# Optimization experiments

Measured on AMD Instinct MI355X. Metric: run time of the kernel, lower is better.

## Reference

```python
import jax, jax.numpy as jnp
import numpy as np

B, T, D, NH, L = 8192, 100, 44, 64, 8  # batch, seq/ode steps, obs_dim, rnn hidden, latent


def setup_inputs() -> dict:
    key = jax.random.key(0)
    ks = jax.random.split(key, 12)
    s = 0.1
    return {
        "x": jax.random.normal(ks[0], (B, T, D), jnp.float32),
        "mask": jax.random.randint(ks[1], (B, T, D), 0, 2).astype(jnp.float32),
        "epsilon": jax.random.normal(ks[2], (B, L), jnp.float32),
        "Wi2h": jax.random.normal(ks[3], (D + NH, NH), jnp.float32) * s,
        "bi2h": jnp.zeros((NH,), jnp.float32),
        "Wh2o": jax.random.normal(ks[4], (NH, 2 * L), jnp.float32) * s,
        "bh2o": jnp.zeros((2 * L,), jnp.float32),
        "Wf1": jax.random.normal(ks[5], (L, NH), jnp.float32) * s,
        "bf1": jnp.zeros((NH,), jnp.float32),
        "Wf2": jax.random.normal(ks[6], (NH, NH), jnp.float32) * s,
        "bf2": jnp.zeros((NH,), jnp.float32),
        "Wf3": jax.random.normal(ks[7], (NH, L), jnp.float32) * s,
        "bf3": jnp.zeros((L,), jnp.float32),
        "Wd1": jax.random.normal(ks[8], (L, NH), jnp.float32) * s,
        "bd1": jnp.zeros((NH,), jnp.float32),
        "Wd2": jax.random.normal(ks[9], (NH, D), jnp.float32) * s,
        "bd2": jnp.zeros((D,), jnp.float32),
    }


def reference(x, mask, epsilon, Wi2h, bi2h, Wh2o, bh2o,
              Wf1, bf1, Wf2, bf2, Wf3, bf3, Wd1, bd1, Wd2, bd2):
    masked_x = x * mask  # [B,T,D]

    # --- reverse-time recognition RNN (scan over time, reversed) ---
    def rnn_step(h, obs):
        h = jnp.tanh(jnp.concatenate([obs, h], axis=1) @ Wi2h + bi2h)
        return h, None

    xs_rev = jnp.transpose(masked_x[:, ::-1, :], (1, 0, 2))  # [T,B,D]
    h0 = jnp.zeros((x.shape[0], Wi2h.shape[1]), x.dtype)
    h_final, _ = jax.lax.scan(rnn_step, h0, xs_rev)
    out = h_final @ Wh2o + bh2o  # [B,2L]
    qz0_mean, qz0_logvar = out[:, :L], out[:, L:]

    # reparameterized latent sample
    z0 = epsilon * jnp.exp(0.5 * qz0_logvar) + qz0_mean  # [B,L]

    # --- latent ODE dynamics, fixed-step RK4 over ts = linspace(0,1,100) ---
    def f(z):
        h1 = jax.nn.elu(z @ Wf1 + bf1)
        h2 = jax.nn.elu(h1 @ Wf2 + bf2)
        return h2 @ Wf3 + bf3

    dt = jnp.asarray(1.0 / (T - 1), x.dtype)

    def rk4_step(z, _):
        k1 = f(z)
        k2 = f(z + 0.5 * dt * k1)
        k3 = f(z + 0.5 * dt * k2)
        k4 = f(z + dt * k3)
        zn = z + (dt / 6.0) * (k1 + 2.0 * k2 + 2.0 * k3 + k4)
        return zn, zn

    _, zs = jax.lax.scan(rk4_step, z0, None, length=T - 1)  # [T-1,B,L]
    pred_z = jnp.transpose(jnp.concatenate([z0[None], zs], axis=0), (1, 0, 2))  # [B,T,L]

    # --- decoder ---
    pred_x = jax.nn.relu(pred_z @ Wd1 + bd1) @ Wd2 + bd2  # [B,T,D]

    # fill observed entries back in
    updated_x = jnp.where(masked_x != 0, masked_x, pred_x)

    # --- loss ---
    noise_logvar = 2.0 * jnp.log(jnp.asarray(0.3, x.dtype))
    log2pi = jnp.log(jnp.asarray(2.0 * np.pi, x.dtype))
    logpx = (-0.5 * (log2pi + noise_logvar +
                     (x - updated_x) ** 2 / jnp.exp(noise_logvar))).sum((-1, -2))  # [B]
    kl = (-0.5 * qz0_logvar + (jnp.exp(qz0_logvar) + qz0_mean ** 2) / 2.0 - 0.5).sum(-1)  # [B]
    loss = jnp.mean(-logpx + kl)
    return loss
```

## Files before the change

kernel.cpp:

```cpp
#include <hip/hip_runtime.h>
#include <stdint.h>


constexpr int B_ = 8192, T_ = 100, D_ = 44, NH_ = 64, L_ = 8;

typedef float f32x4 __attribute__((ext_vector_type(4)));
typedef uint32_t u32x2 __attribute__((ext_vector_type(2)));

#if __has_builtin(__builtin_amdgcn_mfma_f32_16x16x16bf16_1k)
typedef short frag16 __attribute__((ext_vector_type(4)));
#define MFMA16(a, b, c) __builtin_amdgcn_mfma_f32_16x16x16bf16_1k(a, b, c, 0, 0, 0)
#define USE_F16 0
#elif __has_builtin(__builtin_amdgcn_mfma_f32_16x16x16_bf16_1k)
typedef short frag16 __attribute__((ext_vector_type(4)));
#define MFMA16(a, b, c) __builtin_amdgcn_mfma_f32_16x16x16_bf16_1k(a, b, c, 0, 0, 0)
#define USE_F16 0
#elif __has_builtin(__builtin_amdgcn_mfma_f32_16x16x16_bf16)
typedef __bf16 frag16 __attribute__((ext_vector_type(4)));
#define MFMA16(a, b, c) __builtin_amdgcn_mfma_f32_16x16x16_bf16(a, b, c, 0, 0, 0)
#define USE_F16 0
#else
typedef _Float16 frag16 __attribute__((ext_vector_type(4)));
#define MFMA16(a, b, c) __builtin_amdgcn_mfma_f32_16x16x16f16(a, b, c, 0, 0, 0)
#define USE_F16 1
#endif

__device__ __forceinline__ float fexp2(float x) { return __builtin_amdgcn_exp2f(x); }
__device__ __forceinline__ float frcp(float x) { return __builtin_amdgcn_rcpf(x); }
__device__ __forceinline__ float fexp(float x) { return fexp2(x * 1.44269504088896341f); }
__device__ __forceinline__ float tanh_f(float x) {
  float e = fexp2(x * 2.88539008177792681f);
  return 1.0f - 2.0f * frcp(e + 1.0f);
}
__device__ __forceinline__ float elu_f(float x) { return x > 0.0f ? x : (fexp(x) - 1.0f); }

__device__ __forceinline__ uint32_t EW(float v) {
#if USE_F16
  return (uint32_t)__builtin_bit_cast(unsigned short, (_Float16)v);
#else
  return (uint32_t)__builtin_bit_cast(unsigned short, (__bf16)v);
#endif
}
__device__ __forceinline__ uint32_t PK2(float lo, float hi) { return EW(lo) | (EW(hi) << 16); }
__device__ __forceinline__ frag16 fr4(float a, float b, float c, float d) {
  u32x2 u = {PK2(a, b), PK2(c, d)};
  return __builtin_bit_cast(frag16, u);
}
__device__ __forceinline__ frag16 frpk(f32x4 v) {
  u32x2 u = {PK2(v[0], v[1]), PK2(v[2], v[3])};
  return __builtin_bit_cast(frag16, u);
}
__device__ __forceinline__ float f4get(const float4& f, int i) {
  return i == 0 ? f.x : (i == 1 ? f.y : (i == 2 ? f.z : f.w));
}

__global__ __launch_bounds__(128) void fused_kernel(
    const float* __restrict__ x, const float* __restrict__ mask,
    const float* __restrict__ eps,
    const float* __restrict__ Wi2h, const float* __restrict__ bi2h,
    const float* __restrict__ Wh2o, const float* __restrict__ bh2o,
    const float* __restrict__ Wf1, const float* __restrict__ bf1,
    const float* __restrict__ Wf2, const float* __restrict__ bf2,
    const float* __restrict__ Wf3, const float* __restrict__ bf3,
    const float* __restrict__ Wd1, const float* __restrict__ bd1,
    const float* __restrict__ Wd2, const float* __restrict__ bd2,
    float* __restrict__ part) {
  const int tid = threadIdx.x;
  const int wid = tid >> 6;
  const int lane = tid & 63;
  const int c = lane & 15, q = lane >> 4;
  const int r0 = blockIdx.x * 16;
  const f32x4 fzero = {0.f, 0.f, 0.f, 0.f};

  __shared__ __align__(16) uint32_t ring[6400];
  __shared__ uint32_t flags[104];
  __shared__ float sse_sh;

  if (tid < 104) flags[tid] = 0u;
  __syncthreads();

  float klt = 0.0f;

  if (wid == 0) {
    const frag16 fgbias = fr4(1.0f, 0.f, 0.f, 0.f);

    frag16 Ai[4][7];
#pragma unroll
    for (int tau = 0; tau < 4; ++tau)
#pragma unroll
      for (int kc = 0; kc < 7; ++kc) {
        const int m = 16 * tau + c;
        float wv[4];
#pragma unroll
        for (int i = 0; i < 4; ++i) {
          const int k = 16 * kc + 4 * q + i;
          float v = 0.0f;
          if (k < 64) v = Wi2h[(44 + k) * 64 + m];
          else if (k < 108) v = Wi2h[(k - 64) * 64 + m];
          else if (k == 108) v = bi2h[m];
          wv[i] = v;
        }
        Ai[tau][kc] = fr4(wv[0], wv[1], wv[2], wv[3]);
      }
    frag16 Ah2o[4];
#pragma unroll
    for (int kc = 0; kc < 4; ++kc) {
      float wv[4];
#pragma unroll
      for (int i = 0; i < 4; ++i) wv[i] = Wh2o[(16 * kc + 4 * q + i) * 16 + c];
      Ah2o[kc] = fr4(wv[0], wv[1], wv[2], wv[3]);
    }
    f32x4 bo;
#pragma unroll
    for (int r = 0; r < 4; ++r) bo[r] = bh2o[4 * q + r];

    const float* xrowbase = x + (size_t)(r0 + c) * T_ * D_;
    const float* mrowbase = mask + (size_t)(r0 + c) * T_ * D_;

    auto load_obs = [&](int t, float4* xv, float4* mv) {
      const float* xp = xrowbase + (size_t)t * D_;
      const float* mp = mrowbase + (size_t)t * D_;
      xv[0] = *(const float4*)(xp + 4 * q);
      mv[0] = *(const float4*)(mp + 4 * q);
      xv[1] = *(const float4*)(xp + 16 + 4 * q);
      mv[1] = *(const float4*)(mp + 16 + 4 * q);
      float4 zz = {0.f, 0.f, 0.f, 0.f};
      xv[2] = zz; mv[2] = zz;
      if (q < 3) {
        xv[2] = *(const float4*)(xp + 32 + 4 * q);
        mv[2] = *(const float4*)(mp + 32 + 4 * q);
      }
    };
    auto make_ob = [&](const float4* cx, const float4* cm, frag16* ob) {
#pragma unroll
      for (int j = 0; j < 2; ++j) {
        u32x2 u = {PK2(cx[j].x * cm[j].x, cx[j].y * cm[j].y),
                   PK2(cx[j].z * cm[j].z, cx[j].w * cm[j].w)};
        ob[j] = __builtin_bit_cast(frag16, u);
      }
      u32x2 u = {PK2(cx[2].x * cm[2].x, cx[2].y * cm[2].y),
                 PK2(cx[2].z * cm[2].z, cx[2].w * cm[2].w)};
      ob[2] = (q < 3) ? __builtin_bit_cast(frag16, u) : fgbias;
    };

    f32x4 hc[4] = {};
    float4 xo[3], mo[3];
    load_obs(T_ - 1, xo, mo);
    frag16 ob[3];
    make_ob(xo, mo, ob);
    f32x4 pC[4];
#pragma unroll
    for (int tau = 0; tau < 4; ++tau)
      pC[tau] = MFMA16(Ai[tau][6], ob[2],
                       MFMA16(Ai[tau][5], ob[1],
                              MFMA16(Ai[tau][4], ob[0], fzero)));

#pragma unroll 1
    for (int s = 0; s < T_; ++s) {
      const int t = T_ - 1 - s;
      if (t > 0) load_obs(t - 1, xo, mo);

      frag16 bh[4];
#pragma unroll
      for (int tau = 0; tau < 4; ++tau) bh[tau] = frpk(hc[tau]);
#pragma unroll
      for (int tau = 0; tau < 4; ++tau) {
        f32x4 p0 = MFMA16(Ai[tau][0], bh[0], pC[tau]);
        f32x4 p1 = MFMA16(Ai[tau][1], bh[1], fzero);
        f32x4 p2 = MFMA16(Ai[tau][2], bh[2], fzero);
        f32x4 p3 = MFMA16(Ai[tau][3], bh[3], fzero);
#pragma unroll
        for (int r = 0; r < 4; ++r)
          hc[tau][r] = tanh_f((p0[r] + p1[r]) + (p2[r] + p3[r]));
      }

      if (t > 0) {
        make_ob(xo, mo, ob);
#pragma unroll
        for (int tau = 0; tau < 4; ++tau)
          pC[tau] = MFMA16(Ai[tau][6], ob[2],
                           MFMA16(Ai[tau][5], ob[1],
                                  MFMA16(Ai[tau][4], ob[0], fzero)));
      }
    }

    frag16 bhF[4];
#pragma unroll
    for (int tau = 0; tau < 4; ++tau) bhF[tau] = frpk(hc[tau]);
    f32x4 o = bo;
#pragma unroll
    for (int kc = 0; kc < 4; ++kc) o = MFMA16(Ah2o[kc], bhF[kc], o);

    float lv[4];
#pragma unroll
    for (int r = 0; r < 4; ++r)
      lv[r] = __int_as_float(__shfl(__float_as_int(o[r]), lane + 32, 64));

    f32x4 z = {};
    if (q < 2) {
      const float4 ev = *(const float4*)(eps + (size_t)(r0 + c) * 8 + 4 * q);
#pragma unroll
      for (int r = 0; r < 4; ++r) {
        const float m = o[r];
        z[r] = f4get(ev, r) * fexp(0.5f * lv[r]) + m;
        klt += -0.5f * lv[r] + (fexp(lv[r]) + m * m) * 0.5f - 0.5f;
      }
    }
    klt += __shfl_xor(klt, 1);  klt += __shfl_xor(klt, 2);
    klt += __shfl_xor(klt, 4);  klt += __shfl_xor(klt, 8);
    klt += __shfl_xor(klt, 16); klt += __shfl_xor(klt, 32);

    __builtin_amdgcn_sched_barrier(0);

    frag16 A1[4], A2[4][4], A3[4];
#pragma unroll
    for (int tau = 0; tau < 4; ++tau) {
      float w1[4];
#pragma unroll
      for (int i = 0; i < 4; ++i) {
        const int k = 4 * q + i;
        w1[i] = k < 8 ? Wf1[k * 64 + 16 * tau + c] : (k == 8 ? bf1[16 * tau + c] : 0.0f);
      }
      A1[tau] = fr4(w1[0], w1[1], w1[2], w1[3]);
    }
#pragma unroll
    for (int tau = 0; tau < 4; ++tau)
#pragma unroll
      for (int kc = 0; kc < 4; ++kc) {
        float wv[4];
#pragma unroll
        for (int i = 0; i < 4; ++i) wv[i] = Wf2[(16 * kc + 4 * q + i) * 64 + 16 * tau + c];
        A2[tau][kc] = fr4(wv[0], wv[1], wv[2], wv[3]);
      }
#pragma unroll
    for (int kc = 0; kc < 4; ++kc) {
      float wv[4];
#pragma unroll
      for (int i = 0; i < 4; ++i)
        wv[i] = (c < 8) ? Wf3[(16 * kc + 4 * q + i) * 8 + c] : 0.0f;
      A3[kc] = fr4(wv[0], wv[1], wv[2], wv[3]);
    }
    f32x4 b2_[4], b3_;
#pragma unroll
    for (int tau = 0; tau < 4; ++tau)
#pragma unroll
      for (int r = 0; r < 4; ++r) b2_[tau][r] = bf2[16 * tau + 4 * q + r];
#pragma unroll
    for (int r = 0; r < 4; ++r) b3_[r] = (q < 2) ? bf3[4 * q + r] : 0.0f;

    auto build_bz = [&](f32x4 zv) -> frag16 {
      u32x2 u = {PK2(zv[0], zv[1]), PK2(zv[2], zv[3])};
      if (q == 2) { u[0] = EW(1.0f); u[1] = 0u; }
      else if (q == 3) { u[0] = 0u; u[1] = 0u; }
      return __builtin_bit_cast(frag16, u);
    };

    auto feval = [&](frag16 bz) -> f32x4 {
      frag16 bh[4];
#pragma unroll
      for (int tau = 0; tau < 4; ++tau) {
        f32x4 h = MFMA16(A1[tau], bz, fzero);
#pragma unroll
        for (int r = 0; r < 4; ++r) h[r] = elu_f(h[r]);
        bh[tau] = frpk(h);
      }
      frag16 bg[4];
#pragma unroll
      for (int tau = 0; tau < 4; ++tau) {
        f32x4 g0 = MFMA16(A2[tau][0], bh[0], b2_[tau]);
        f32x4 g1 = MFMA16(A2[tau][1], bh[1], fzero);
        f32x4 g2 = MFMA16(A2[tau][2], bh[2], fzero);
        f32x4 g3 = MFMA16(A2[tau][3], bh[3], fzero);
        f32x4 g;
#pragma unroll
        for (int r = 0; r < 4; ++r) g[r] = elu_f((g0[r] + g1[r]) + (g2[r] + g3[r]));
        bg[tau] = frpk(g);
      }
      f32x4 r0_ = MFMA16(A3[0], bg[0], b3_);
      f32x4 r1_ = MFMA16(A3[1], bg[1], fzero);
      f32x4 r2_ = MFMA16(A3[2], bg[2], fzero);
      f32x4 r3_ = MFMA16(A3[3], bg[3], fzero);
      f32x4 rr;
#pragma unroll
      for (int r = 0; r < 4; ++r) rr[r] = (r0_[r] + r1_[r]) + (r2_[r] + r3_[r]);
      return rr;
    };

    const float dt = 1.0f / (float)(T_ - 1);
    const float hdt = 0.5f * dt;

#pragma unroll 1
    for (int t = 0; t < T_; ++t) {
      if (q < 2) {
        u32x2 v = {PK2(z[0], z[1]), PK2(z[2], z[3])};
        *(u32x2*)(ring + (t * 32 + c * 2 + q) * 2) = v;
      }
      asm volatile("" ::: "memory");
      if (lane == 0) ((volatile uint32_t*)flags)[t] = 1u;

      if (t < T_ - 1) {
        f32x4 k1 = feval(build_bz(z));
        f32x4 zt;
#pragma unroll
        for (int r = 0; r < 4; ++r) zt[r] = z[r] + hdt * k1[r];
        f32x4 k2 = feval(build_bz(zt));
#pragma unroll
        for (int r = 0; r < 4; ++r) zt[r] = z[r] + hdt * k2[r];
        f32x4 k3 = feval(build_bz(zt));
#pragma unroll
        for (int r = 0; r < 4; ++r) zt[r] = z[r] + dt * k3[r];
        f32x4 k4 = feval(build_bz(zt));
#pragma unroll
        for (int r = 0; r < 4; ++r)
          z[r] += (dt / 6.0f) * (k1[r] + 2.0f * (k2[r] + k3[r]) + k4[r]);
      }
    }
  } else {
    frag16 Ad1[4], Ad2[3][4];
#pragma unroll
    for (int tau = 0; tau < 4; ++tau) {
      float wd[4];
#pragma unroll
      for (int i = 0; i < 4; ++i) {
        const int k = 4 * q + i;
        wd[i] = k < 8 ? Wd1[k * 64 + 16 * tau + c] : (k == 8 ? bd1[16 * tau + c] : 0.0f);
      }
      Ad1[tau] = fr4(wd[0], wd[1], wd[2], wd[3]);
    }
#pragma unroll
    for (int tau = 0; tau < 3; ++tau)
#pragma unroll
      for (int kc = 0; kc < 4; ++kc) {
        const int m = 16 * tau + c;
        float wv[4];
#pragma unroll
        for (int i = 0; i < 4; ++i)
          wv[i] = (m < 44) ? Wd2[(16 * kc + 4 * q + i) * 44 + m] : 0.0f;
        Ad2[tau][kc] = fr4(wv[0], wv[1], wv[2], wv[3]);
      }
    f32x4 bd2_[3];
#pragma unroll
    for (int tau = 0; tau < 3; ++tau)
#pragma unroll
      for (int r = 0; r < 4; ++r) {
        const int d = 16 * tau + 4 * q + r;
        bd2_[tau][r] = (d < 44) ? bd2[d] : 0.0f;
      }

    float qacc = 0.0f;
    volatile uint32_t* vf = flags;

#pragma unroll 1
    for (int t = 0; t < T_; ++t) {
      float4 xc[3], mc[3];
#pragma unroll
      for (int tau = 0; tau < 3; ++tau) {
        const int d0 = 16 * tau + 4 * q;
        if (d0 < 44) {
          const size_t off = (size_t)(r0 + c) * T_ * D_ + (size_t)t * D_ + d0;
          xc[tau] = *(const float4*)(x + off);
          mc[tau] = *(const float4*)(mask + off);
        } else {
          float4 zz = {0.f, 0.f, 0.f, 0.f};
          xc[tau] = zz; mc[tau] = zz;
        }
      }

      while (vf[t] == 0u) __builtin_amdgcn_s_sleep(1);
      asm volatile("" ::: "memory");

      frag16 bz;
      {
        u32x2 u = {0u, 0u};
        if (q < 2) u = *(const u32x2*)(ring + (t * 32 + c * 2 + q) * 2);
        else if (q == 2) u[0] = EW(1.0f);
        bz = __builtin_bit_cast(frag16, u);
      }

      frag16 bhd[4];
#pragma unroll
      for (int tau = 0; tau < 4; ++tau) {
        f32x4 hd = MFMA16(Ad1[tau], bz, fzero);
#pragma unroll
        for (int r = 0; r < 4; ++r) hd[r] = fmaxf(hd[r], 0.0f);
        bhd[tau] = frpk(hd);
      }
#pragma unroll
      for (int tau = 0; tau < 3; ++tau) {
        f32x4 p0 = MFMA16(Ad2[tau][0], bhd[0], bd2_[tau]);
        f32x4 p1 = MFMA16(Ad2[tau][1], bhd[1], fzero);
        f32x4 p2 = MFMA16(Ad2[tau][2], bhd[2], fzero);
        f32x4 p3 = MFMA16(Ad2[tau][3], bhd[3], fzero);
        if (16 * tau + 4 * q < 44) {
#pragma unroll
          for (int r = 0; r < 4; ++r) {
            const float p = (p0[r] + p1[r]) + (p2[r] + p3[r]);
            const float xa = f4get(xc[tau], r), ma = f4get(mc[tau], r);
            const float mx = xa * ma;
            const float upd = (mx != 0.0f) ? mx : p;
            const float df = xa - upd;
            qacc += df * df;
          }
        }
      }
    }

    float tot = qacc * (0.5f / 0.09f);
    tot += __shfl_xor(tot, 1);  tot += __shfl_xor(tot, 2);
    tot += __shfl_xor(tot, 4);  tot += __shfl_xor(tot, 8);
    tot += __shfl_xor(tot, 16); tot += __shfl_xor(tot, 32);
    if (lane == 0) sse_sh = tot;
  }

  __syncthreads();
  if (tid == 0) part[blockIdx.x] = sse_sh + klt;
}

__global__ __launch_bounds__(512) void reduce_kernel(const float* __restrict__ part,
                                                     float* __restrict__ out) {
  __shared__ float s[8];
  const int tid = threadIdx.x;
  float v = part[tid];
  v += __shfl_xor(v, 1);  v += __shfl_xor(v, 2);
  v += __shfl_xor(v, 4);  v += __shfl_xor(v, 8);
  v += __shfl_xor(v, 16); v += __shfl_xor(v, 32);
  if ((tid & 63) == 0) s[tid >> 6] = v;
  __syncthreads();
  if (tid == 0) {
    float acc = 0.0f;
#pragma unroll
    for (int i = 0; i < 8; ++i) acc += s[i];
    const float c0 = 0.28503427112126353f;
    out[0] = acc * (1.0f / (float)B_) - (float)(T_ * D_) * c0;
  }
}

extern "C" void kernel_launch(void* const* d_in, const int* in_sizes, int n_in,
                              void* d_out, int out_size, void* d_ws, size_t ws_size,
                              hipStream_t stream) {
  const float* x    = (const float*)d_in[0];
  const float* mask = (const float*)d_in[1];
  const float* eps  = (const float*)d_in[2];
  const float* Wi2h = (const float*)d_in[3];
  const float* bi2h = (const float*)d_in[4];
  const float* Wh2o = (const float*)d_in[5];
  const float* bh2o = (const float*)d_in[6];
  const float* Wf1  = (const float*)d_in[7];
  const float* bf1  = (const float*)d_in[8];
  const float* Wf2  = (const float*)d_in[9];
  const float* bf2  = (const float*)d_in[10];
  const float* Wf3  = (const float*)d_in[11];
  const float* bf3  = (const float*)d_in[12];
  const float* Wd1  = (const float*)d_in[13];
  const float* bd1  = (const float*)d_in[14];
  const float* Wd2  = (const float*)d_in[15];
  const float* bd2  = (const float*)d_in[16];

  float* loss = (float*)d_out;
  float* part = (float*)d_ws;

  fused_kernel<<<dim3(B_ / 16), dim3(128), 0, stream>>>(
      x, mask, eps, Wi2h, bi2h, Wh2o, bh2o, Wf1, bf1, Wf2, bf2, Wf3, bf3,
      Wd1, bd1, Wd2, bd2, part);
  reduce_kernel<<<dim3(1), dim3(512), 0, stream>>>(part, loss);
}
```

Before: 698.1 us.

## Process two 16-row tiles per block to interleave independent MFMA chains

```diff
diff --git a/kernel.cpp b/kernel.cpp
--- a/kernel.cpp
+++ b/kernel.cpp
@@ -69,10 +69,10 @@
   const int wid = tid >> 6;
   const int lane = tid & 63;
   const int c = lane & 15, q = lane >> 4;
-  const int r0 = blockIdx.x * 16;
+  const int r0 = blockIdx.x * 32;
   const f32x4 fzero = {0.f, 0.f, 0.f, 0.f};
 
-  __shared__ __align__(16) uint32_t ring[6400];
+  __shared__ __align__(16) uint32_t ring[12800];
   __shared__ uint32_t flags[104];
   __shared__ float sse_sh;
 
@@ -114,12 +114,16 @@
 #pragma unroll
     for (int r = 0; r < 4; ++r) bo[r] = bh2o[4 * q + r];
 
-    const float* xrowbase = x + (size_t)(r0 + c) * T_ * D_;
-    const float* mrowbase = mask + (size_t)(r0 + c) * T_ * D_;
-
-    auto load_obs = [&](int t, float4* xv, float4* mv) {
-      const float* xp = xrowbase + (size_t)t * D_;
-      const float* mp = mrowbase + (size_t)t * D_;
+    const float* xrb[2], * mrb[2];
+#pragma unroll
+    for (int it = 0; it < 2; ++it) {
+      xrb[it] = x + (size_t)(r0 + 16 * it + c) * T_ * D_;
+      mrb[it] = mask + (size_t)(r0 + 16 * it + c) * T_ * D_;
+    }
+
+    auto load_obs = [&](int it, int t, float4* xv, float4* mv) {
+      const float* xp = xrb[it] + (size_t)t * D_;
+      const float* mp = mrb[it] + (size_t)t * D_;
       xv[0] = *(const float4*)(xp + 4 * q);
       mv[0] = *(const float4*)(mp + 4 * q);
       xv[1] = *(const float4*)(xp + 16 + 4 * q);
@@ -143,68 +147,93 @@
       ob[2] = (q < 3) ? __builtin_bit_cast(frag16, u) : fgbias;
     };
 
-    f32x4 hc[4] = {};
-    float4 xo[3], mo[3];
-    load_obs(T_ - 1, xo, mo);
-    frag16 ob[3];
-    make_ob(xo, mo, ob);
-    f32x4 pC[4];
+    f32x4 hc[2][4] = {};
+    float4 xo[2][3], mo[2][3];
+    frag16 ob[2][3];
+    f32x4 pC[2][4];
+#pragma unroll
+    for (int it = 0; it < 2; ++it) {
+      load_obs(it, T_ - 1, xo[it], mo[it]);
+      make_ob(xo[it], mo[it], ob[it]);
+    }
 #pragma unroll
     for (int tau = 0; tau < 4; ++tau)
-      pC[tau] = MFMA16(Ai[tau][6], ob[2],
-                       MFMA16(Ai[tau][5], ob[1],
-                              MFMA16(Ai[tau][4], ob[0], fzero)));
+#pragma unroll
+      for (int it = 0; it < 2; ++it)
+        pC[it][tau] = MFMA16(Ai[tau][6], ob[it][2],
+                             MFMA16(Ai[tau][5], ob[it][1],
+                                    MFMA16(Ai[tau][4], ob[it][0], fzero)));
 
 #pragma unroll 1
     for (int s = 0; s < T_; ++s) {
       const int t = T_ - 1 - s;
-      if (t > 0) load_obs(t - 1, xo, mo);
-
-      frag16 bh[4];
-#pragma unroll
-      for (int tau = 0; tau < 4; ++tau) bh[tau] = frpk(hc[tau]);
+      if (t > 0) {
+#pragma unroll
+        for (int it = 0; it < 2; ++it) load_obs(it, t - 1, xo[it], mo[it]);
+      }
+
+      frag16 bh[2][4];
+#pragma unroll
+      for (int tau = 0; tau < 4; ++tau)
+#pragma unroll
+        for (int it = 0; it < 2; ++it) bh[it][tau] = frpk(hc[it][tau]);
 #pragma unroll
       for (int tau = 0; tau < 4; ++tau) {
-        f32x4 p0 = MFMA16(Ai[tau][0], bh[0], pC[tau]);
-        f32x4 p1 = MFMA16(Ai[tau][1], bh[1], fzero);
-        f32x4 p2 = MFMA16(Ai[tau][2], bh[2], fzero);
-        f32x4 p3 = MFMA16(Ai[tau][3], bh[3], fzero);
-#pragma unroll
-        for (int r = 0; r < 4; ++r)
-          hc[tau][r] = tanh_f((p0[r] + p1[r]) + (p2[r] + p3[r]));
+        f32x4 p0[2], p1[2], p2[2], p3[2];
+#pragma unroll
+        for (int it = 0; it < 2; ++it) p0[it] = MFMA16(Ai[tau][0], bh[it][0], pC[it][tau]);
+#pragma unroll
+        for (int it = 0; it < 2; ++it) p1[it] = MFMA16(Ai[tau][1], bh[it][1], fzero);
+#pragma unroll
+        for (int it = 0; it < 2; ++it) p2[it] = MFMA16(Ai[tau][2], bh[it][2], fzero);
+#pragma unroll
+        for (int it = 0; it < 2; ++it) p3[it] = MFMA16(Ai[tau][3], bh[it][3], fzero);
+#pragma unroll
+        for (int it = 0; it < 2; ++it)
+#pragma unroll
+          for (int r = 0; r < 4; ++r)
+            hc[it][tau][r] = tanh_f((p0[it][r] + p1[it][r]) + (p2[it][r] + p3[it][r]));
       }
 
       if (t > 0) {
-        make_ob(xo, mo, ob);
+#pragma unroll
+        for (int it = 0; it < 2; ++it) make_ob(xo[it], mo[it], ob[it]);
 #pragma unroll
         for (int tau = 0; tau < 4; ++tau)
-          pC[tau] = MFMA16(Ai[tau][6], ob[2],
-                           MFMA16(Ai[tau][5], ob[1],
-                                  MFMA16(Ai[tau][4], ob[0], fzero)));
-      }
-    }
-
-    frag16 bhF[4];
-#pragma unroll
-    for (int tau = 0; tau < 4; ++tau) bhF[tau] = frpk(hc[tau]);
-    f32x4 o = bo;
-#pragma unroll
-    for (int kc = 0; kc < 4; ++kc) o = MFMA16(Ah2o[kc], bhF[kc], o);
-
-    float lv[4];
-#pragma unroll
-    for (int r = 0; r < 4; ++r)
-      lv[r] = __int_as_float(__shfl(__float_as_int(o[r]), lane + 32, 64));
-
-    f32x4 z = {};
-    if (q < 2) {
-      const float4 ev = *(const float4*)(eps + (size_t)(r0 + c) * 8 + 4 * q);
-#pragma unroll
-      for (int r = 0; r < 4; ++r) {
-        const float m = o[r];
-        z[r] = f4get(ev, r) * fexp(0.5f * lv[r]) + m;
-        klt += -0.5f * lv[r] + (fexp(lv[r]) + m * m) * 0.5f - 0.5f;
-      }
+#pragma unroll
+          for (int it = 0; it < 2; ++it)
+            pC[it][tau] = MFMA16(Ai[tau][6], ob[it][2],
+                                 MFMA16(Ai[tau][5], ob[it][1],
+                                        MFMA16(Ai[tau][4], ob[it][0], fzero)));
+      }
+    }
+
+    f32x4 z[2];
+#pragma unroll
+    for (int it = 0; it < 2; ++it) {
+      frag16 bhF[4];
+#pragma unroll
+      for (int tau = 0; tau < 4; ++tau) bhF[tau] = frpk(hc[it][tau]);
+      f32x4 o = bo;
+#pragma unroll
+      for (int kc = 0; kc < 4; ++kc) o = MFMA16(Ah2o[kc], bhF[kc], o);
+
+      float lv[4];
+#pragma unroll
+      for (int r = 0; r < 4; ++r)
+        lv[r] = __int_as_float(__shfl(__float_as_int(o[r]), lane + 32, 64));
+
+      f32x4 zt = {};
+      if (q < 2) {
+        const float4 ev = *(const float4*)(eps + (size_t)(r0 + 16 * it + c) * 8 + 4 * q);
+#pragma unroll
+        for (int r = 0; r < 4; ++r) {
+          const float m = o[r];
+          zt[r] = f4get(ev, r) * fexp(0.5f * lv[r]) + m;
+          klt += -0.5f * lv[r] + (fexp(lv[r]) + m * m) * 0.5f - 0.5f;
+        }
+      }
+      z[it] = zt;
     }
     klt += __shfl_xor(klt, 1);  klt += __shfl_xor(klt, 2);
     klt += __shfl_xor(klt, 4);  klt += __shfl_xor(klt, 8);
@@ -255,35 +284,56 @@
       return __builtin_bit_cast(frag16, u);
     };
 
-    auto feval = [&](frag16 bz) -> f32x4 {
-      frag16 bh[4];
+    auto feval2 = [&](frag16 bzA, frag16 bzB, f32x4* kk) {
+      frag16 bz[2] = {bzA, bzB};
+      frag16 bh[2][4];
 #pragma unroll
       for (int tau = 0; tau < 4; ++tau) {
-        f32x4 h = MFMA16(A1[tau], bz, fzero);
-#pragma unroll
-        for (int r = 0; r < 4; ++r) h[r] = elu_f(h[r]);
-        bh[tau] = frpk(h);
-      }
-      frag16 bg[4];
+        f32x4 h[2];
+#pragma unroll
+        for (int it = 0; it < 2; ++it) h[it] = MFMA16(A1[tau], bz[it], fzero);
+#pragma unroll
+        for (int it = 0; it < 2; ++it) {
+#pragma unroll
+          for (int r = 0; r < 4; ++r) h[it][r] = elu_f(h[it][r]);
+          bh[it][tau] = frpk(h[it]);
+        }
+      }
+      frag16 bg[2][4];
 #pragma unroll
       for (int tau = 0; tau < 4; ++tau) {
-        f32x4 g0 = MFMA16(A2[tau][0], bh[0], b2_[tau]);
-        f32x4 g1 = MFMA16(A2[tau][1], bh[1], fzero);
-        f32x4 g2 = MFMA16(A2[tau][2], bh[2], fzero);
-        f32x4 g3 = MFMA16(A2[tau][3], bh[3], fzero);
-        f32x4 g;
-#pragma unroll
-        for (int r = 0; r < 4; ++r) g[r] = elu_f((g0[r] + g1[r]) + (g2[r] + g3[r]));
-        bg[tau] = frpk(g);
-      }
-      f32x4 r0_ = MFMA16(A3[0], bg[0], b3_);
-      f32x4 r1_ = MFMA16(A3[1], bg[1], fzero);
-      f32x4 r2_ = MFMA16(A3[2], bg[2], fzero);
-      f32x4 r3_ = MFMA16(A3[3], bg[3], fzero);
-      f32x4 rr;
-#pragma unroll
-      for (int r = 0; r < 4; ++r) rr[r] = (r0_[r] + r1_[r]) + (r2_[r] + r3_[r]);
-      return rr;
+        f32x4 g0[2], g1[2], g2[2], g3[2];
+#pragma unroll
+        for (int it = 0; it < 2; ++it) g0[it] = MFMA16(A2[tau][0], bh[it][0], b2_[tau]);
+#pragma unroll
+        for (int it = 0; it < 2; ++it) g1[it] = MFMA16(A2[tau][1], bh[it][1], fzero);
+#pragma unroll
+        for (int it = 0; it < 2; ++it) g2[it] = MFMA16(A2[tau][2], bh[it][2], fzero);
+#pragma unroll
+        for (int it = 0; it < 2; ++it) g3[it] = MFMA16(A2[tau][3], bh[it][3], fzero);
+#pragma unroll
+        for (int it = 0; it < 2; ++it) {
+          f32x4 g;
+#pragma unroll
+          for (int r = 0; r < 4; ++r)
+            g[r] = elu_f((g0[it][r] + g1[it][r]) + (g2[it][r] + g3[it][r]));
+          bg[it][tau] = frpk(g);
+        }
+      }
+      f32x4 r0_[2], r1_[2], r2_[2], r3_[2];
+#pragma unroll
+      for (int it = 0; it < 2; ++it) r0_[it] = MFMA16(A3[0], bg[it][0], b3_);
+#pragma unroll
+      for (int it = 0; it < 2; ++it) r1_[it] = MFMA16(A3[1], bg[it][1], fzero);
+#pragma unroll
+      for (int it = 0; it < 2; ++it) r2_[it] = MFMA16(A3[2], bg[it][2], fzero);
+#pragma unroll
+      for (int it = 0; it < 2; ++it) r3_[it] = MFMA16(A3[3], bg[it][3], fzero);
+#pragma unroll
+      for (int it = 0; it < 2; ++it)
+#pragma unroll
+        for (int r = 0; r < 4; ++r)
+          kk[it][r] = (r0_[it][r] + r1_[it][r]) + (r2_[it][r] + r3_[it][r]);
     };
 
     const float dt = 1.0f / (float)(T_ - 1);
@@ -292,27 +342,38 @@
 #pragma unroll 1
     for (int t = 0; t < T_; ++t) {
       if (q < 2) {
-        u32x2 v = {PK2(z[0], z[1]), PK2(z[2], z[3])};
-        *(u32x2*)(ring + (t * 32 + c * 2 + q) * 2) = v;
+#pragma unroll
+        for (int it = 0; it < 2; ++it) {
+          u32x2 v = {PK2(z[it][0], z[it][1]), PK2(z[it][2], z[it][3])};
+          *(u32x2*)(ring + (t * 64 + it * 32 + c * 2 + q) * 2) = v;
+        }
       }
       asm volatile("" ::: "memory");
       if (lane == 0) ((volatile uint32_t*)flags)[t] = 1u;
 
       if (t < T_ - 1) {
-        f32x4 k1 = feval(build_bz(z));
-        f32x4 zt;
-#pragma unroll
-        for (int r = 0; r < 4; ++r) zt[r] = z[r] + hdt * k1[r];
-        f32x4 k2 = feval(build_bz(zt));
-#pragma unroll
-        for (int r = 0; r < 4; ++r) zt[r] = z[r] + hdt * k2[r];
-        f32x4 k3 = feval(build_bz(zt));
-#pragma unroll
-        for (int r = 0; r < 4; ++r) zt[r] = z[r] + dt * k3[r];
-        f32x4 k4 = feval(build_bz(zt));
-#pragma unroll
-        for (int r = 0; r < 4; ++r)
-          z[r] += (dt / 6.0f) * (k1[r] + 2.0f * (k2[r] + k3[r]) + k4[r]);
+        f32x4 k1[2], k2[2], k3[2], k4[2], zt[2];
+        feval2(build_bz(z[0]), build_bz(z[1]), k1);
+#pragma unroll
+        for (int it = 0; it < 2; ++it)
+#pragma unroll
+          for (int r = 0; r < 4; ++r) zt[it][r] = z[it][r] + hdt * k1[it][r];
+        feval2(build_bz(zt[0]), build_bz(zt[1]), k2);
+#pragma unroll
+        for (int it = 0; it < 2; ++it)
+#pragma unroll
+          for (int r = 0; r < 4; ++r) zt[it][r] = z[it][r] + hdt * k2[it][r];
+        feval2(build_bz(zt[0]), build_bz(zt[1]), k3);
+#pragma unroll
+        for (int it = 0; it < 2; ++it)
+#pragma unroll
+          for (int r = 0; r < 4; ++r) zt[it][r] = z[it][r] + dt * k3[it][r];
+        feval2(build_bz(zt[0]), build_bz(zt[1]), k4);
+#pragma unroll
+        for (int it = 0; it < 2; ++it)
+#pragma unroll
+          for (int r = 0; r < 4; ++r)
+            z[it][r] += (dt / 6.0f) * (k1[it][r] + 2.0f * (k2[it][r] + k3[it][r]) + k4[it][r]);
       }
     }
   } else {
@@ -352,55 +413,70 @@
 
 #pragma unroll 1
     for (int t = 0; t < T_; ++t) {
-      float4 xc[3], mc[3];
-#pragma unroll
-      for (int tau = 0; tau < 3; ++tau) {
-        const int d0 = 16 * tau + 4 * q;
-        if (d0 < 44) {
-          const size_t off = (size_t)(r0 + c) * T_ * D_ + (size_t)t * D_ + d0;
-          xc[tau] = *(const float4*)(x + off);
-          mc[tau] = *(const float4*)(mask + off);
-        } else {
-          float4 zz = {0.f, 0.f, 0.f, 0.f};
-          xc[tau] = zz; mc[tau] = zz;
-        }
-      }
+      float4 xc[2][3], mc[2][3];
+#pragma unroll
+      for (int it = 0; it < 2; ++it)
+#pragma unroll
+        for (int tau = 0; tau < 3; ++tau) {
+          const int d0 = 16 * tau + 4 * q;
+          if (d0 < 44) {
+            const size_t off = (size_t)(r0 + 16 * it + c) * T_ * D_ + (size_t)t * D_ + d0;
+            xc[it][tau] = *(const float4*)(x + off);
+            mc[it][tau] = *(const float4*)(mask + off);
+          } else {
+            float4 zz = {0.f, 0.f, 0.f, 0.f};
+            xc[it][tau] = zz; mc[it][tau] = zz;
+          }
+        }
 
       while (vf[t] == 0u) __builtin_amdgcn_s_sleep(1);
       asm volatile("" ::: "memory");
 
-      frag16 bz;
-      {
+      frag16 bz[2];
+#pragma unroll
+      for (int it = 0; it < 2; ++it) {
         u32x2 u = {0u, 0u};
-        if (q < 2) u = *(const u32x2*)(ring + (t * 32 + c * 2 + q) * 2);
+        if (q < 2) u = *(const u32x2*)(ring + (t * 64 + it * 32 + c * 2 + q) * 2);
         else if (q == 2) u[0] = EW(1.0f);
-        bz = __builtin_bit_cast(frag16, u);
-      }
-
-      frag16 bhd[4];
+        bz[it] = __builtin_bit_cast(frag16, u);
+      }
+
+      frag16 bhd[2][4];
 #pragma unroll
       for (int tau = 0; tau < 4; ++tau) {
-        f32x4 hd = MFMA16(Ad1[tau], bz, fzero);
-#pragma unroll
-        for (int r = 0; r < 4; ++r) hd[r] = fmaxf(hd[r], 0.0f);
-        bhd[tau] = frpk(hd);
+        f32x4 hd[2];
+#pragma unroll
+        for (int it = 0; it < 2; ++it) hd[it] = MFMA16(Ad1[tau], bz[it], fzero);
+#pragma unroll
+        for (int it = 0; it < 2; ++it) {
+#pragma unroll
+          for (int r = 0; r < 4; ++r) hd[it][r] = fmaxf(hd[it][r], 0.0f);
+          bhd[it][tau] = frpk(hd[it]);
+        }
       }
 #pragma unroll
       for (int tau = 0; tau < 3; ++tau) {
-        f32x4 p0 = MFMA16(Ad2[tau][0], bhd[0], bd2_[tau]);
-        f32x4 p1 = MFMA16(Ad2[tau][1], bhd[1], fzero);
-        f32x4 p2 = MFMA16(Ad2[tau][2], bhd[2], fzero);
-        f32x4 p3 = MFMA16(Ad2[tau][3], bhd[3], fzero);
+        f32x4 p0[2], p1[2], p2[2], p3[2];
+#pragma unroll
+        for (int it = 0; it < 2; ++it) p0[it] = MFMA16(Ad2[tau][0], bhd[it][0], bd2_[tau]);
+#pragma unroll
+        for (int it = 0; it < 2; ++it) p1[it] = MFMA16(Ad2[tau][1], bhd[it][1], fzero);
+#pragma unroll
+        for (int it = 0; it < 2; ++it) p2[it] = MFMA16(Ad2[tau][2], bhd[it][2], fzero);
+#pragma unroll
+        for (int it = 0; it < 2; ++it) p3[it] = MFMA16(Ad2[tau][3], bhd[it][3], fzero);
         if (16 * tau + 4 * q < 44) {
 #pragma unroll
-          for (int r = 0; r < 4; ++r) {
-            const float p = (p0[r] + p1[r]) + (p2[r] + p3[r]);
-            const float xa = f4get(xc[tau], r), ma = f4get(mc[tau], r);
-            const float mx = xa * ma;
-            const float upd = (mx != 0.0f) ? mx : p;
-            const float df = xa - upd;
-            qacc += df * df;
-          }
+          for (int it = 0; it < 2; ++it)
+#pragma unroll
+            for (int r = 0; r < 4; ++r) {
+              const float p = (p0[it][r] + p1[it][r]) + (p2[it][r] + p3[it][r]);
+              const float xa = f4get(xc[it][tau], r), ma = f4get(mc[it][tau], r);
+              const float mx = xa * ma;
+              const float upd = (mx != 0.0f) ? mx : p;
+              const float df = xa - upd;
+              qacc += df * df;
+            }
         }
       }
     }
@@ -416,9 +492,9 @@
   if (tid == 0) part[blockIdx.x] = sse_sh + klt;
 }
 
-__global__ __launch_bounds__(512) void reduce_kernel(const float* __restrict__ part,
+__global__ __launch_bounds__(256) void reduce_kernel(const float* __restrict__ part,
                                                      float* __restrict__ out) {
-  __shared__ float s[8];
+  __shared__ float s[4];
   const int tid = threadIdx.x;
   float v = part[tid];
   v += __shfl_xor(v, 1);  v += __shfl_xor(v, 2);
@@ -429,7 +505,7 @@
   if (tid == 0) {
     float acc = 0.0f;
 #pragma unroll
-    for (int i = 0; i < 8; ++i) acc += s[i];
+    for (int i = 0; i < 4; ++i) acc += s[i];
     const float c0 = 0.28503427112126353f;
     out[0] = acc * (1.0f / (float)B_) - (float)(T_ * D_) * c0;
   }
@@ -459,8 +535,8 @@
   float* loss = (float*)d_out;
   float* part = (float*)d_ws;
 
-  fused_kernel<<<dim3(B_ / 16), dim3(128), 0, stream>>>(
+  fused_kernel<<<dim3(B_ / 32), dim3(128), 0, stream>>>(
       x, mask, eps, Wi2h, bi2h, Wh2o, bh2o, Wf1, bf1, Wf2, bf2, Wf3, bf3,
       Wd1, bd1, Wd2, bd2, part);
-  reduce_kernel<<<dim3(1), dim3(512), 0, stream>>>(part, loss);
-}
+  reduce_kernel<<<dim3(1), dim3(256), 0, stream>>>(part, loss);
+}
```

After: 1.077 ms. 54.3% more time.

## Offload RNN input projection to decoder wave via LDS ring buffer

Applied to the files above, without the earlier changes.

```diff
diff --git a/kernel.cpp b/kernel.cpp
--- a/kernel.cpp
+++ b/kernel.cpp
@@ -73,46 +73,237 @@
   const f32x4 fzero = {0.f, 0.f, 0.f, 0.f};
 
   __shared__ __align__(16) uint32_t ring[6400];
+  __shared__ __align__(16) float pcring[8192];
   __shared__ uint32_t flags[104];
+  __shared__ uint32_t w1prog;
+  __shared__ uint32_t w0cons;
   __shared__ float sse_sh;
 
   if (tid < 104) flags[tid] = 0u;
+  if (tid == 0) { w1prog = 0u; w0cons = 0u; }
   __syncthreads();
 
   float klt = 0.0f;
 
   if (wid == 0) {
-    const frag16 fgbias = fr4(1.0f, 0.f, 0.f, 0.f);
-
-    frag16 Ai[4][7];
+    frag16 Ah[4][4];
 #pragma unroll
     for (int tau = 0; tau < 4; ++tau)
 #pragma unroll
-      for (int kc = 0; kc < 7; ++kc) {
+      for (int kc = 0; kc < 4; ++kc) {
         const int m = 16 * tau + c;
         float wv[4];
 #pragma unroll
+        for (int i = 0; i < 4; ++i) wv[i] = Wi2h[(44 + 16 * kc + 4 * q + i) * 64 + m];
+        Ah[tau][kc] = fr4(wv[0], wv[1], wv[2], wv[3]);
+      }
+    frag16 Ah2o[4];
+#pragma unroll
+    for (int kc = 0; kc < 4; ++kc) {
+      float wv[4];
+#pragma unroll
+      for (int i = 0; i < 4; ++i) wv[i] = Wh2o[(16 * kc + 4 * q + i) * 16 + c];
+      Ah2o[kc] = fr4(wv[0], wv[1], wv[2], wv[3]);
+    }
+    f32x4 bo;
+#pragma unroll
+    for (int r = 0; r < 4; ++r) bo[r] = bh2o[4 * q + r];
+
+    volatile uint32_t* vprod = &w1prog;
+    volatile uint32_t* vcons = &w0cons;
+
+    while (*vprod < 1u) __builtin_amdgcn_s_sleep(1);
+    asm volatile("" ::: "memory");
+    f32x4 pcur[4], pnext[4];
+#pragma unroll
+    for (int tau = 0; tau < 4; ++tau)
+      pcur[tau] = *(const f32x4*)(pcring + tau * 256 + lane * 4);
+    if (lane == 0) *vcons = 1u;
+
+    f32x4 hc[4] = {};
+#pragma unroll 1
+    for (int s = 0; s < T_; ++s) {
+      if ((s & 3) == 0) {
+        const uint32_t need = (uint32_t)((s + 5 > T_) ? T_ : s + 5);
+        while (*vprod < need) __builtin_amdgcn_s_sleep(1);
+        asm volatile("" ::: "memory");
+      }
+      if (s < T_ - 1) {
+        const int sl = (s + 1) & 7;
+#pragma unroll
+        for (int tau = 0; tau < 4; ++tau)
+          pnext[tau] = *(const f32x4*)(pcring + sl * 1024 + tau * 256 + lane * 4);
+        if (lane == 0) *vcons = (uint32_t)(s + 2);
+      }
+
+      frag16 bh[4];
+#pragma unroll
+      for (int tau = 0; tau < 4; ++tau) bh[tau] = frpk(hc[tau]);
+#pragma unroll
+      for (int tau = 0; tau < 4; ++tau) {
+        f32x4 p0 = MFMA16(Ah[tau][0], bh[0], pcur[tau]);
+        f32x4 p1 = MFMA16(Ah[tau][1], bh[1], fzero);
+        f32x4 p2 = MFMA16(Ah[tau][2], bh[2], fzero);
+        f32x4 p3 = MFMA16(Ah[tau][3], bh[3], fzero);
+#pragma unroll
+        for (int r = 0; r < 4; ++r)
+          hc[tau][r] = tanh_f((p0[r] + p1[r]) + (p2[r] + p3[r]));
+      }
+#pragma unroll
+      for (int tau = 0; tau < 4; ++tau) pcur[tau] = pnext[tau];
+    }
+
+    frag16 bhF[4];
+#pragma unroll
+    for (int tau = 0; tau < 4; ++tau) bhF[tau] = frpk(hc[tau]);
+    f32x4 o = bo;
+#pragma unroll
+    for (int kc = 0; kc < 4; ++kc) o = MFMA16(Ah2o[kc], bhF[kc], o);
+
+    float lv[4];
+#pragma unroll
+    for (int r = 0; r < 4; ++r)
+      lv[r] = __int_as_float(__shfl(__float_as_int(o[r]), lane + 32, 64));
+
+    f32x4 z = {};
+    if (q < 2) {
+      const float4 ev = *(const float4*)(eps + (size_t)(r0 + c) * 8 + 4 * q);
+#pragma unroll
+      for (int r = 0; r < 4; ++r) {
+        const float m = o[r];
+        z[r] = f4get(ev, r) * fexp(0.5f * lv[r]) + m;
+        klt += -0.5f * lv[r] + (fexp(lv[r]) + m * m) * 0.5f - 0.5f;
+      }
+    }
+    klt += __shfl_xor(klt, 1);  klt += __shfl_xor(klt, 2);
+    klt += __shfl_xor(klt, 4);  klt += __shfl_xor(klt, 8);
+    klt += __shfl_xor(klt, 16); klt += __shfl_xor(klt, 32);
+
+    __builtin_amdgcn_sched_barrier(0);
+
+    frag16 A1[4], A2[4][4], A3[4];
+#pragma unroll
+    for (int tau = 0; tau < 4; ++tau) {
+      float w1[4];
+#pragma unroll
+      for (int i = 0; i < 4; ++i) {
+        const int k = 4 * q + i;
+        w1[i] = k < 8 ? Wf1[k * 64 + 16 * tau + c] : (k == 8 ? bf1[16 * tau + c] : 0.0f);
+      }
+      A1[tau] = fr4(w1[0], w1[1], w1[2], w1[3]);
+    }
+#pragma unroll
+    for (int tau = 0; tau < 4; ++tau)
+#pragma unroll
+      for (int kc = 0; kc < 4; ++kc) {
+        float wv[4];
+#pragma unroll
+        for (int i = 0; i < 4; ++i) wv[i] = Wf2[(16 * kc + 4 * q + i) * 64 + 16 * tau + c];
+        A2[tau][kc] = fr4(wv[0], wv[1], wv[2], wv[3]);
+      }
+#pragma unroll
+    for (int kc = 0; kc < 4; ++kc) {
+      float wv[4];
+#pragma unroll
+      for (int i = 0; i < 4; ++i)
+        wv[i] = (c < 8) ? Wf3[(16 * kc + 4 * q + i) * 8 + c] : 0.0f;
+      A3[kc] = fr4(wv[0], wv[1], wv[2], wv[3]);
+    }
+    f32x4 b2_[4], b3_;
+#pragma unroll
+    for (int tau = 0; tau < 4; ++tau)
+#pragma unroll
+      for (int r = 0; r < 4; ++r) b2_[tau][r] = bf2[16 * tau + 4 * q + r];
+#pragma unroll
+    for (int r = 0; r < 4; ++r) b3_[r] = (q < 2) ? bf3[4 * q + r] : 0.0f;
+
+    auto build_bz = [&](f32x4 zv) -> frag16 {
+      u32x2 u = {PK2(zv[0], zv[1]), PK2(zv[2], zv[3])};
+      if (q == 2) { u[0] = EW(1.0f); u[1] = 0u; }
+      else if (q == 3) { u[0] = 0u; u[1] = 0u; }
+      return __builtin_bit_cast(frag16, u);
+    };
+
+    auto feval = [&](frag16 bz) -> f32x4 {
+      frag16 bh[4];
+#pragma unroll
+      for (int tau = 0; tau < 4; ++tau) {
+        f32x4 h = MFMA16(A1[tau], bz, fzero);
+#pragma unroll
+        for (int r = 0; r < 4; ++r) h[r] = elu_f(h[r]);
+        bh[tau] = frpk(h);
+      }
+      frag16 bg[4];
+#pragma unroll
+      for (int tau = 0; tau < 4; ++tau) {
+        f32x4 g0 = MFMA16(A2[tau][0], bh[0], b2_[tau]);
+        f32x4 g1 = MFMA16(A2[tau][1], bh[1], fzero);
+        f32x4 g2 = MFMA16(A2[tau][2], bh[2], fzero);
+        f32x4 g3 = MFMA16(A2[tau][3], bh[3], fzero);
+        f32x4 g;
+#pragma unroll
+        for (int r = 0; r < 4; ++r) g[r] = elu_f((g0[r] + g1[r]) + (g2[r] + g3[r]));
+        bg[tau] = frpk(g);
+      }
+      f32x4 r0_ = MFMA16(A3[0], bg[0], b3_);
+      f32x4 r1_ = MFMA16(A3[1], bg[1], fzero);
+      f32x4 r2_ = MFMA16(A3[2], bg[2], fzero);
+      f32x4 r3_ = MFMA16(A3[3], bg[3], fzero);
+      f32x4 rr;
+#pragma unroll
+      for (int r = 0; r < 4; ++r) rr[r] = (r0_[r] + r1_[r]) + (r2_[r] + r3_[r]);
+      return rr;
+    };
+
+    const float dt = 1.0f / (float)(T_ - 1);
+    const float hdt = 0.5f * dt;
+
+#pragma unroll 1
+    for (int t = 0; t < T_; ++t) {
+      if (q < 2) {
+        u32x2 v = {PK2(z[0], z[1]), PK2(z[2], z[3])};
+        *(u32x2*)(ring + (t * 32 + c * 2 + q) * 2) = v;
+      }
+      asm volatile("" ::: "memory");
+      if (lane == 0) ((volatile uint32_t*)flags)[t] = 1u;
+
+      if (t < T_ - 1) {
+        f32x4 k1 = feval(build_bz(z));
+        f32x4 zt;
+#pragma unroll
+        for (int r = 0; r < 4; ++r) zt[r] = z[r] + hdt * k1[r];
+        f32x4 k2 = feval(build_bz(zt));
+#pragma unroll
+        for (int r = 0; r < 4; ++r) zt[r] = z[r] + hdt * k2[r];
+        f32x4 k3 = feval(build_bz(zt));
+#pragma unroll
+        for (int r = 0; r < 4; ++r) zt[r] = z[r] + dt * k3[r];
+        f32x4 k4 = feval(build_bz(zt));
+#pragma unroll
+        for (int r = 0; r < 4; ++r)
+          z[r] += (dt / 6.0f) * (k1[r] + 2.0f * (k2[r] + k3[r]) + k4[r]);
+      }
+    }
+  } else {
+    const frag16 fgbias = fr4(1.0f, 0.f, 0.f, 0.f);
+
+    frag16 Ao[4][3];
+#pragma unroll
+    for (int tau = 0; tau < 4; ++tau)
+#pragma unroll
+      for (int kc = 0; kc < 3; ++kc) {
+        const int m = 16 * tau + c;
+        float wv[4];
+#pragma unroll
         for (int i = 0; i < 4; ++i) {
-          const int k = 16 * kc + 4 * q + i;
+          const int k = 64 + 16 * kc + 4 * q + i;
           float v = 0.0f;
-          if (k < 64) v = Wi2h[(44 + k) * 64 + m];
-          else if (k < 108) v = Wi2h[(k - 64) * 64 + m];
+          if (k < 108) v = Wi2h[(k - 64) * 64 + m];
           else if (k == 108) v = bi2h[m];
           wv[i] = v;
         }
-        Ai[tau][kc] = fr4(wv[0], wv[1], wv[2], wv[3]);
-      }
-    frag16 Ah2o[4];
-#pragma unroll
-    for (int kc = 0; kc < 4; ++kc) {
-      float wv[4];
-#pragma unroll
-      for (int i = 0; i < 4; ++i) wv[i] = Wh2o[(16 * kc + 4 * q + i) * 16 + c];
-      Ah2o[kc] = fr4(wv[0], wv[1], wv[2], wv[3]);
-    }
-    f32x4 bo;
-#pragma unroll
-    for (int r = 0; r < 4; ++r) bo[r] = bh2o[4 * q + r];
+        Ao[tau][kc] = fr4(wv[0], wv[1], wv[2], wv[3]);
+      }
 
     const float* xrowbase = x + (size_t)(r0 + c) * T_ * D_;
     const float* mrowbase = mask + (size_t)(r0 + c) * T_ * D_;
@@ -143,179 +334,40 @@
       ob[2] = (q < 3) ? __builtin_bit_cast(frag16, u) : fgbias;
     };
 
-    f32x4 hc[4] = {};
-    float4 xo[3], mo[3];
-    load_obs(T_ - 1, xo, mo);
-    frag16 ob[3];
-    make_ob(xo, mo, ob);
-    f32x4 pC[4];
-#pragma unroll
-    for (int tau = 0; tau < 4; ++tau)
-      pC[tau] = MFMA16(Ai[tau][6], ob[2],
-                       MFMA16(Ai[tau][5], ob[1],
-                              MFMA16(Ai[tau][4], ob[0], fzero)));
-
+    volatile uint32_t* vcons = &w0cons;
+    volatile uint32_t* vprod = &w1prog;
+
+    {
+      float4 xo[3], mo[3];
+      load_obs(T_ - 1, xo, mo);
 #pragma unroll 1
-    for (int s = 0; s < T_; ++s) {
-      const int t = T_ - 1 - s;
-      if (t > 0) load_obs(t - 1, xo, mo);
-
-      frag16 bh[4];
-#pragma unroll
-      for (int tau = 0; tau < 4; ++tau) bh[tau] = frpk(hc[tau]);
-#pragma unroll
-      for (int tau = 0; tau < 4; ++tau) {
-        f32x4 p0 = MFMA16(Ai[tau][0], bh[0], pC[tau]);
-        f32x4 p1 = MFMA16(Ai[tau][1], bh[1], fzero);
-        f32x4 p2 = MFMA16(Ai[tau][2], bh[2], fzero);
-        f32x4 p3 = MFMA16(Ai[tau][3], bh[3], fzero);
-#pragma unroll
-        for (int r = 0; r < 4; ++r)
-          hc[tau][r] = tanh_f((p0[r] + p1[r]) + (p2[r] + p3[r]));
-      }
-
-      if (t > 0) {
-        make_ob(xo, mo, ob);
+      for (int s1 = 0; s1 < T_; ++s1) {
+        const int t = T_ - 1 - s1;
+        float4 cx[3], cm[3];
+#pragma unroll
+        for (int j = 0; j < 3; ++j) { cx[j] = xo[j]; cm[j] = mo[j]; }
+        if (t > 0) load_obs(t - 1, xo, mo);
+
+        frag16 ob[3];
+        make_ob(cx, cm, ob);
+        f32x4 pc[4];
 #pragma unroll
         for (int tau = 0; tau < 4; ++tau)
-          pC[tau] = MFMA16(Ai[tau][6], ob[2],
-                           MFMA16(Ai[tau][5], ob[1],
-                                  MFMA16(Ai[tau][4], ob[0], fzero)));
-      }
-    }
-
-    frag16 bhF[4];
-#pragma unroll
-    for (int tau = 0; tau < 4; ++tau) bhF[tau] = frpk(hc[tau]);
-    f32x4 o = bo;
-#pragma unroll
-    for (int kc = 0; kc < 4; ++kc) o = MFMA16(Ah2o[kc], bhF[kc], o);
-
-    float lv[4];
-#pragma unroll
-    for (int r = 0; r < 4; ++r)
-      lv[r] = __int_as_float(__shfl(__float_as_int(o[r]), lane + 32, 64));
-
-    f32x4 z = {};
-    if (q < 2) {
-      const float4 ev = *(const float4*)(eps + (size_t)(r0 + c) * 8 + 4 * q);
-#pragma unroll
-      for (int r = 0; r < 4; ++r) {
-        const float m = o[r];
-        z[r] = f4get(ev, r) * fexp(0.5f * lv[r]) + m;
-        klt += -0.5f * lv[r] + (fexp(lv[r]) + m * m) * 0.5f - 0.5f;
-      }
-    }
-    klt += __shfl_xor(klt, 1);  klt += __shfl_xor(klt, 2);
-    klt += __shfl_xor(klt, 4);  klt += __shfl_xor(klt, 8);
-    klt += __shfl_xor(klt, 16); klt += __shfl_xor(klt, 32);
-
-    __builtin_amdgcn_sched_barrier(0);
-
-    frag16 A1[4], A2[4][4], A3[4];
-#pragma unroll
-    for (int tau = 0; tau < 4; ++tau) {
-      float w1[4];
-#pragma unroll
-      for (int i = 0; i < 4; ++i) {
-        const int k = 4 * q + i;
-        w1[i] = k < 8 ? Wf1[k * 64 + 16 * tau + c] : (k == 8 ? bf1[16 * tau + c] : 0.0f);
-      }
-      A1[tau] = fr4(w1[0], w1[1], w1[2], w1[3]);
-    }
-#pragma unroll
-    for (int tau = 0; tau < 4; ++tau)
-#pragma unroll
-      for (int kc = 0; kc < 4; ++kc) {
-        float wv[4];
-#pragma unroll
-        for (int i = 0; i < 4; ++i) wv[i] = Wf2[(16 * kc + 4 * q + i) * 64 + 16 * tau + c];
-        A2[tau][kc] = fr4(wv[0], wv[1], wv[2], wv[3]);
-      }
-#pragma unroll
-    for (int kc = 0; kc < 4; ++kc) {
-      float wv[4];
-#pragma unroll
-      for (int i = 0; i < 4; ++i)
-        wv[i] = (c < 8) ? Wf3[(16 * kc + 4 * q + i) * 8 + c] : 0.0f;
-      A3[kc] = fr4(wv[0], wv[1], wv[2], wv[3]);
-    }
-    f32x4 b2_[4], b3_;
-#pragma unroll
-    for (int tau = 0; tau < 4; ++tau)
-#pragma unroll
-      for (int r = 0; r < 4; ++r) b2_[tau][r] = bf2[16 * tau + 4 * q + r];
-#pragma unroll
-    for (int r = 0; r < 4; ++r) b3_[r] = (q < 2) ? bf3[4 * q + r] : 0.0f;
-
-    auto build_bz = [&](f32x4 zv) -> frag16 {
-      u32x2 u = {PK2(zv[0], zv[1]), PK2(zv[2], zv[3])};
-      if (q == 2) { u[0] = EW(1.0f); u[1] = 0u; }
-      else if (q == 3) { u[0] = 0u; u[1] = 0u; }
-      return __builtin_bit_cast(frag16, u);
-    };
-
-    auto feval = [&](frag16 bz) -> f32x4 {
-      frag16 bh[4];
-#pragma unroll
-      for (int tau = 0; tau < 4; ++tau) {
-        f32x4 h = MFMA16(A1[tau], bz, fzero);
-#pragma unroll
-        for (int r = 0; r < 4; ++r) h[r] = elu_f(h[r]);
-        bh[tau] = frpk(h);
-      }
-      frag16 bg[4];
-#pragma unroll
-      for (int tau = 0; tau < 4; ++tau) {
-        f32x4 g0 = MFMA16(A2[tau][0], bh[0], b2_[tau]);
-        f32x4 g1 = MFMA16(A2[tau][1], bh[1], fzero);
-        f32x4 g2 = MFMA16(A2[tau][2], bh[2], fzero);
-        f32x4 g3 = MFMA16(A2[tau][3], bh[3], fzero);
-        f32x4 g;
-#pragma unroll
-        for (int r = 0; r < 4; ++r) g[r] = elu_f((g0[r] + g1[r]) + (g2[r] + g3[r]));
-        bg[tau] = frpk(g);
-      }
-      f32x4 r0_ = MFMA16(A3[0], bg[0], b3_);
-      f32x4 r1_ = MFMA16(A3[1], bg[1], fzero);
-      f32x4 r2_ = MFMA16(A3[2], bg[2], fzero);
-      f32x4 r3_ = MFMA16(A3[3], bg[3], fzero);
-      f32x4 rr;
-#pragma unroll
-      for (int r = 0; r < 4; ++r) rr[r] = (r0_[r] + r1_[r]) + (r2_[r] + r3_[r]);
-      return rr;
-    };
-
-    const float dt = 1.0f / (float)(T_ - 1);
-    const float hdt = 0.5f * dt;
-
-#pragma unroll 1
-    for (int t = 0; t < T_; ++t) {
-      if (q < 2) {
-        u32x2 v = {PK2(z[0], z[1]), PK2(z[2], z[3])};
-        *(u32x2*)(ring + (t * 32 + c * 2 + q) * 2) = v;
-      }
-      asm volatile("" ::: "memory");
-      if (lane == 0) ((volatile uint32_t*)flags)[t] = 1u;
-
-      if (t < T_ - 1) {
-        f32x4 k1 = feval(build_bz(z));
-        f32x4 zt;
-#pragma unroll
-        for (int r = 0; r < 4; ++r) zt[r] = z[r] + hdt * k1[r];
-        f32x4 k2 = feval(build_bz(zt));
-#pragma unroll
-        for (int r = 0; r < 4; ++r) zt[r] = z[r] + hdt * k2[r];
-        f32x4 k3 = feval(build_bz(zt));
-#pragma unroll
-        for (int r = 0; r < 4; ++r) zt[r] = z[r] + dt * k3[r];
-        f32x4 k4 = feval(build_bz(zt));
-#pragma unroll
-        for (int r = 0; r < 4; ++r)
-          z[r] += (dt / 6.0f) * (k1[r] + 2.0f * (k2[r] + k3[r]) + k4[r]);
-      }
-    }
-  } else {
+          pc[tau] = MFMA16(Ao[tau][2], ob[2],
+                           MFMA16(Ao[tau][1], ob[1],
+                                  MFMA16(Ao[tau][0], ob[0], fzero)));
+
+        while ((uint32_t)s1 >= *vcons + 8u) __builtin_amdgcn_s_sleep(1);
+        asm volatile("" ::: "memory");
+        const int sl = s1 & 7;
+#pragma unroll
+        for (int tau = 0; tau < 4; ++tau)
+          *(f32x4*)(pcring + sl * 1024 + tau * 256 + lane * 4) = pc[tau];
+        asm volatile("" ::: "memory");
+        if (lane == 0) *vprod = (uint32_t)(s1 + 1);
+      }
+    }
+
     frag16 Ad1[4], Ad2[3][4];
 #pragma unroll
     for (int tau = 0; tau < 4; ++tau) {
```

After: 681.2 us. 2.4% less time.
